# Kernel tuning notes

Hardware: AMD Instinct MI355X
Metric: run time of the kernel (lower is better)

Reference implementation:

```python
import jax, jax.numpy as jnp
import numpy as np

N_NODES = 100000
N_EDGES = 1600000
D_FEAT = 64
COS_EPS = 1e-8  # torch.nn.functional.cosine_similarity default eps


def setup_inputs() -> dict:
    key = jax.random.key(0)
    k1, k2 = jax.random.split(key)
    features = jax.random.normal(k1, (N_NODES, D_FEAT), dtype=jnp.float32)
    edge_index = jax.random.randint(k2, (2, N_EDGES), 0, N_NODES, dtype=jnp.int64)
    return {"features": features, "edge_index": edge_index}


def _mean_agg(h, src, dst, n_nodes):
    # copy_u: message = h[src]; fn.mean: per-dst mean over incoming messages
    msg_sum = jax.ops.segment_sum(h[src], dst, num_segments=n_nodes)  # [N, d]
    deg = jax.ops.segment_sum(jnp.ones(src.shape, h.dtype), dst, num_segments=n_nodes)  # [N]
    deg = deg[:, None]
    # nodes with zero in-degree get 0 (DGL mean semantics)
    return jnp.where(deg > 0, msg_sum / jnp.maximum(deg, 1.0), 0.0)


def reference(features, edge_index):
    src, dst = edge_index[0], edge_index[1]
    n = features.shape[0]
    x1 = _mean_agg(features, src, dst, n)   # gcn1
    x2 = _mean_agg(x1, src, dst, n)         # gcn2
    # cosine similarity along feature dim
    dot = jnp.sum(x1 * x2, axis=-1)
    n1 = jnp.linalg.norm(x1, axis=-1)
    n2 = jnp.linalg.norm(x2, axis=-1)
    cos = dot / jnp.maximum(n1 * n2, COS_EPS)
    w = cos[:, None]
    return w * x2 + (1.0 - w) * x1
```

## Files before the change

kernel.cpp:

```cpp
#include <hip/hip_runtime.h>
#include <hip/hip_fp16.h>
#include <math.h>

#define N_NODES 100000
#define N_EDGES 1600000
#define D_FEAT  64

#define NPB     256
#define NBC     ((N_NODES + NPB - 1) / NPB)
#define F1_WGS  512
#define NV4     (N_EDGES / 4)
#define CHUNK_V ((NV4 + F1_WGS - 1) / F1_WGS)
#define STAGE_CAP 8192
#define CASTN   ((N_NODES * D_FEAT) / 4)
#define CAST_BLOCKS ((CASTN + 255) / 256)


__device__ __forceinline__ uint4 pack8(const float* v) {
    __half2 h0 = __floats2half2_rn(v[0], v[1]);
    __half2 h1 = __floats2half2_rn(v[2], v[3]);
    __half2 h2 = __floats2half2_rn(v[4], v[5]);
    __half2 h3 = __floats2half2_rn(v[6], v[7]);
    uint4 st;
    st.x = *(unsigned*)&h0; st.y = *(unsigned*)&h1;
    st.z = *(unsigned*)&h2; st.w = *(unsigned*)&h3;
    return st;
}

__device__ __forceinline__ void unp8(uint4 u, float* a) {
    { __half2 h = *(__half2*)&u.x; float2 f = __half22float2(h); a[0]=f.x; a[1]=f.y; }
    { __half2 h = *(__half2*)&u.y; float2 f = __half22float2(h); a[2]=f.x; a[3]=f.y; }
    { __half2 h = *(__half2*)&u.z; float2 f = __half22float2(h); a[4]=f.x; a[5]=f.y; }
    { __half2 h = *(__half2*)&u.w; float2 f = __half22float2(h); a[6]=f.x; a[7]=f.y; }
}

__device__ __forceinline__ int block_excl_scan_512(int v, int t, int* wsum) {
    int lane = t & 63, wv = t >> 6;
    int incl = v;
    #pragma unroll
    for (int m = 1; m < 64; m <<= 1) {
        int o = __shfl_up(incl, m);
        if (lane >= m) incl += o;
    }
    if (lane == 63) wsum[wv] = incl;
    __syncthreads();
    int prefix = 0;
    #pragma unroll
    for (int j = 0; j < 8; j++)
        if (j < wv) prefix += wsum[j];
    return prefix + incl - v;
}


__global__ void cast_and_hist(const float* __restrict__ feat,
                              __half* __restrict__ feat_h,
                              const int4* __restrict__ dst4,
                              int* __restrict__ percnt) {
    if (blockIdx.x >= F1_WGS) {
        int i = (blockIdx.x - F1_WGS) * 256 + threadIdx.x;
        if (i < CASTN) {
            float4 v = ((const float4*)feat)[i];
            __half2 h0 = __floats2half2_rn(v.x, v.y);
            __half2 h1 = __floats2half2_rn(v.z, v.w);
            uint2 st;
            st.x = *(unsigned*)&h0;
            st.y = *(unsigned*)&h1;
            ((uint2*)feat_h)[i] = st;
        }
        return;
    }
    __shared__ int cnt[NBC];
    for (int i = threadIdx.x; i < NBC; i += blockDim.x) cnt[i] = 0;
    __syncthreads();
    int i0 = blockIdx.x * CHUNK_V;
    int i1 = min(i0 + CHUNK_V, NV4);
    for (int i = i0 + threadIdx.x; i < i1; i += blockDim.x) {
        int4 d = dst4[i];
        atomicAdd(&cnt[d.x >> 8], 1);
        atomicAdd(&cnt[d.y >> 8], 1);
        atomicAdd(&cnt[d.z >> 8], 1);
        atomicAdd(&cnt[d.w >> 8], 1);
    }
    __syncthreads();
    for (int i = threadIdx.x; i < NBC; i += blockDim.x)
        percnt[i * F1_WGS + blockIdx.x] = cnt[i];
}


__global__ __launch_bounds__(F1_WGS) void bucket_colscan(
        int* __restrict__ percnt, int* __restrict__ bhist) {
    __shared__ int wsum[8];
    int b = blockIdx.x, t = threadIdx.x;
    int v = percnt[b * F1_WGS + t];
    int excl = block_excl_scan_512(v, t, wsum);
    percnt[b * F1_WGS + t] = excl;
    if (t == F1_WGS - 1) bhist[b] = excl + v;
}

__global__ __launch_bounds__(F1_WGS) void bucketize(
        const int4* __restrict__ src4,
        const int4* __restrict__ dst4,
        const int* __restrict__ bhist,
        const int* __restrict__ percnt,
        unsigned int* __restrict__ tmp1) {
    __shared__ int base[NBC];
    __shared__ int cur[NBC];
    __shared__ int wsum[8];
    int wg = blockIdx.x, t = threadIdx.x;
    int v = (t < NBC) ? bhist[t] : 0;
    int excl = block_excl_scan_512(v, t, wsum);
    if (t < NBC) {
        base[t] = excl + percnt[t * F1_WGS + wg];
        cur[t] = 0;
    }
    __syncthreads();
    int i0 = wg * CHUNK_V;
    int i1 = min(i0 + CHUNK_V, NV4);
    for (int i = i0 + t; i < i1; i += F1_WGS) {
        int4 d = dst4[i];
        int4 s = src4[i];
        {
            int b = d.x >> 8; int r = atomicAdd(&cur[b], 1);
            tmp1[base[b] + r] = ((unsigned)s.x << 8) | (unsigned)(d.x & 255);
        }
        {
            int b = d.y >> 8; int r = atomicAdd(&cur[b], 1);
            tmp1[base[b] + r] = ((unsigned)s.y << 8) | (unsigned)(d.y & 255);
        }
        {
            int b = d.z >> 8; int r = atomicAdd(&cur[b], 1);
            tmp1[base[b] + r] = ((unsigned)s.z << 8) | (unsigned)(d.z & 255);
        }
        {
            int b = d.w >> 8; int r = atomicAdd(&cur[b], 1);
            tmp1[base[b] + r] = ((unsigned)s.w << 8) | (unsigned)(d.w & 255);
        }
    }
}

__global__ __launch_bounds__(512) void bucket_csr(
        const unsigned int* __restrict__ tmp1,
        const int* __restrict__ bhist,
        int* __restrict__ offsets,
        int* __restrict__ csr_src) {
    __shared__ int cnt[NPB];
    __shared__ int off[NPB];
    __shared__ int wsum[8];
    __shared__ int stage[STAGE_CAP];
    __shared__ int sEbase, sEcnt;
    int b = blockIdx.x, t = threadIdx.x;

    {
        int v = (t < NBC) ? bhist[t] : 0;
        int ex = block_excl_scan_512(v, t, wsum);
        if (t == b) { sEbase = ex; sEcnt = v; }
    }
    if (t < NPB) cnt[t] = 0;
    __syncthreads();
    int ebase = sEbase;
    int ecnt  = sEcnt;
    int node0 = b * NPB;

    for (int i = t; i < ecnt; i += 512)
        atomicAdd(&cnt[tmp1[ebase + i] & 255], 1);
    __syncthreads();

    int v = (t < NPB) ? cnt[t] : 0;
    int excl = block_excl_scan_512(v, t, wsum);
    if (t < NPB) {
        off[t] = excl;
        cnt[t] = 0;
        if (node0 + t < N_NODES) offsets[node0 + t] = ebase + excl;
    }
    if (b == NBC - 1 && t == 0) offsets[N_NODES] = N_EDGES;
    __syncthreads();

    if (ecnt <= STAGE_CAP) {
        for (int i = t; i < ecnt; i += 512) {
            unsigned u = tmp1[ebase + i];
            int d = (int)(u & 255);
            int r = atomicAdd(&cnt[d], 1);
            stage[off[d] + r] = (int)(u >> 8);
        }
        __syncthreads();
        for (int i = t; i < ecnt; i += 512)
            csr_src[ebase + i] = stage[i];
    } else {
        for (int i = t; i < ecnt; i += 512) {
            unsigned u = tmp1[ebase + i];
            int d = (int)(u & 255);
            int r = atomicAdd(&cnt[d], 1);
            csr_src[ebase + off[d] + r] = (int)(u >> 8);
        }
    }
}


__global__ void gather1_kernel(const __half* __restrict__ feat_h,
                               const int* __restrict__ offsets,
                               const int* __restrict__ csr,
                               __half* __restrict__ x1_h) {
    __shared__ int scsr[4][64];
    int wv = threadIdx.x >> 6;
    int node = blockIdx.x * 4 + wv;
    if (node >= N_NODES) return;
    int lane = threadIdx.x & 63;
    int g = lane >> 3;
    int fid = (lane & 7) * 8;

    int base = offsets[node];
    int deg = offsets[node + 1] - base;

    if (lane < deg) scsr[wv][lane] = csr[base + lane];
    __builtin_amdgcn_wave_barrier();

    __half2 h0 = __float2half2_rn(0.f), h1 = h0, h2 = h0, h3 = h0;
    int dmax = min(deg, 64);
    for (int j = g; j < dmax; j += 8) {
        int s = scsr[wv][j];
        uint4 u = *(const uint4*)(feat_h + ((size_t)s << 6) + fid);
        h0 = __hadd2(h0, *(__half2*)&u.x);
        h1 = __hadd2(h1, *(__half2*)&u.y);
        h2 = __hadd2(h2, *(__half2*)&u.z);
        h3 = __hadd2(h3, *(__half2*)&u.w);
    }
    for (int j = 64 + g; j < deg; j += 8) {
        int s = csr[base + j];
        uint4 u = *(const uint4*)(feat_h + ((size_t)s << 6) + fid);
        h0 = __hadd2(h0, *(__half2*)&u.x);
        h1 = __hadd2(h1, *(__half2*)&u.y);
        h2 = __hadd2(h2, *(__half2*)&u.z);
        h3 = __hadd2(h3, *(__half2*)&u.w);
    }
    float acc[8];
    { float2 f = __half22float2(h0); acc[0]=f.x; acc[1]=f.y; }
    { float2 f = __half22float2(h1); acc[2]=f.x; acc[3]=f.y; }
    { float2 f = __half22float2(h2); acc[4]=f.x; acc[5]=f.y; }
    { float2 f = __half22float2(h3); acc[6]=f.x; acc[7]=f.y; }
    #pragma unroll
    for (int m = 8; m < 64; m <<= 1)
        #pragma unroll
        for (int t = 0; t < 8; t++)
            acc[t] += __shfl_xor(acc[t], m);

    if (lane < 8) {
        float inv = (deg > 0) ? 1.0f / (float)deg : 0.0f;
        float r[8];
        #pragma unroll
        for (int t = 0; t < 8; t++) r[t] = acc[t] * inv;
        *(uint4*)(x1_h + ((size_t)node << 6) + fid) = pack8(r);
    }
}

__global__ void gather2_finalize_kernel(const __half* __restrict__ x1_h,
                                        const int* __restrict__ offsets,
                                        const int* __restrict__ csr,
                                        float* __restrict__ out) {
    __shared__ int scsr[4][64];
    int wv = threadIdx.x >> 6;
    int node = blockIdx.x * 4 + wv;
    if (node >= N_NODES) return;
    int lane = threadIdx.x & 63;
    int g = lane >> 3;
    int fid = (lane & 7) * 8;

    int base = offsets[node];
    int deg = offsets[node + 1] - base;

    if (lane < deg) scsr[wv][lane] = csr[base + lane];
    __builtin_amdgcn_wave_barrier();

    __half2 h0 = __float2half2_rn(0.f), h1 = h0, h2 = h0, h3 = h0;
    int dmax = min(deg, 64);
    for (int j = g; j < dmax; j += 8) {
        int s = scsr[wv][j];
        uint4 u = *(const uint4*)(x1_h + ((size_t)s << 6) + fid);
        h0 = __hadd2(h0, *(__half2*)&u.x);
        h1 = __hadd2(h1, *(__half2*)&u.y);
        h2 = __hadd2(h2, *(__half2*)&u.z);
        h3 = __hadd2(h3, *(__half2*)&u.w);
    }
    for (int j = 64 + g; j < deg; j += 8) {
        int s = csr[base + j];
        uint4 u = *(const uint4*)(x1_h + ((size_t)s << 6) + fid);
        h0 = __hadd2(h0, *(__half2*)&u.x);
        h1 = __hadd2(h1, *(__half2*)&u.y);
        h2 = __hadd2(h2, *(__half2*)&u.z);
        h3 = __hadd2(h3, *(__half2*)&u.w);
    }
    float acc[8];
    { float2 f = __half22float2(h0); acc[0]=f.x; acc[1]=f.y; }
    { float2 f = __half22float2(h1); acc[2]=f.x; acc[3]=f.y; }
    { float2 f = __half22float2(h2); acc[4]=f.x; acc[5]=f.y; }
    { float2 f = __half22float2(h3); acc[6]=f.x; acc[7]=f.y; }
    #pragma unroll
    for (int m = 8; m < 64; m <<= 1)
        #pragma unroll
        for (int t = 0; t < 8; t++)
            acc[t] += __shfl_xor(acc[t], m);

    float inv = (deg > 0) ? 1.0f / (float)deg : 0.0f;
    float b[8], a[8];
    #pragma unroll
    for (int t = 0; t < 8; t++) b[t] = acc[t] * inv;

    uint4 ua = *(const uint4*)(x1_h + ((size_t)node << 6) + fid);
    unp8(ua, a);

    float dot = 0.f, nn1 = 0.f, nn2 = 0.f;
    #pragma unroll
    for (int t = 0; t < 8; t++) {
        dot += a[t] * b[t];
        nn1 += a[t] * a[t];
        nn2 += b[t] * b[t];
    }
    #pragma unroll
    for (int m = 1; m < 64; m <<= 1) {
        dot += __shfl_xor(dot, m);
        nn1 += __shfl_xor(nn1, m);
        nn2 += __shfl_xor(nn2, m);
    }
    dot *= 0.125f; nn1 *= 0.125f; nn2 *= 0.125f;

    float w = dot / fmaxf(sqrtf(nn1) * sqrtf(nn2), 1e-8f);
    if (lane < 8) {
        float omw = 1.0f - w;
        float4 r0, r1;
        r0.x = w*b[0] + omw*a[0]; r0.y = w*b[1] + omw*a[1];
        r0.z = w*b[2] + omw*a[2]; r0.w = w*b[3] + omw*a[3];
        r1.x = w*b[4] + omw*a[4]; r1.y = w*b[5] + omw*a[5];
        r1.z = w*b[6] + omw*a[6]; r1.w = w*b[7] + omw*a[7];
        float* po = out + ((size_t)node << 6) + fid;
        *(float4*)po = r0;
        *(float4*)(po + 4) = r1;
    }
}


extern "C" void kernel_launch(void* const* d_in, const int* in_sizes, int n_in,
                              void* d_out, int out_size, void* d_ws, size_t ws_size,
                              hipStream_t stream) {
    const float* feat = (const float*)d_in[0];
    const int*   eidx = (const int*)d_in[1];
    const int4*  src4 = (const int4*)eidx;
    const int4*  dst4 = (const int4*)(eidx + N_EDGES);

    __half*       feat_h  = (__half*)d_ws;
    __half*       x1_h    = feat_h + (size_t)N_NODES * D_FEAT;
    unsigned int* tmp1    = (unsigned int*)(x1_h + (size_t)N_NODES * D_FEAT);
    int*          csr_src = (int*)(tmp1 + N_EDGES);
    int*          offsets = csr_src + N_EDGES;
    int*          percnt  = offsets + (N_NODES + 1);
    int*          bhist   = percnt + NBC * F1_WGS;
    float*        out     = (float*)d_out;

    cast_and_hist <<<F1_WGS + CAST_BLOCKS, 256, 0, stream>>>(feat, feat_h, dst4, percnt);
    bucket_colscan<<<NBC, F1_WGS, 0, stream>>>(percnt, bhist);
    bucketize     <<<F1_WGS, F1_WGS, 0, stream>>>(src4, dst4, bhist, percnt, tmp1);
    bucket_csr    <<<NBC, 512, 0, stream>>>(tmp1, bhist, offsets, csr_src);

    const int BLK = 256;
    int nblocks = (N_NODES + 3) / 4;
    gather1_kernel<<<nblocks, BLK, 0, stream>>>(feat_h, offsets, csr_src, x1_h);
    gather2_finalize_kernel<<<nblocks, BLK, 0, stream>>>(x1_h, offsets, csr_src, out);
}
```

Before: 196.9 us.

## Map eight nodes per wavefront in gather kernels, removing cross-group shuffle reductions

```diff
diff --git a/kernel.cpp b/kernel.cpp
--- a/kernel.cpp
+++ b/kernel.cpp
@@ -14,6 +14,8 @@
 #define STAGE_CAP 8192
 #define CASTN   ((N_NODES * D_FEAT) / 4)
 #define CAST_BLOCKS ((CASTN + 255) / 256)
+
+#define GCAP    68
 
 
 __device__ __forceinline__ uint4 pack8(const float* v) {
@@ -196,115 +198,102 @@
 }
 
 
-__global__ void gather1_kernel(const __half* __restrict__ feat_h,
-                               const int* __restrict__ offsets,
-                               const int* __restrict__ csr,
-                               __half* __restrict__ x1_h) {
-    __shared__ int scsr[4][64];
-    int wv = threadIdx.x >> 6;
-    int node = blockIdx.x * 4 + wv;
-    if (node >= N_NODES) return;
+__global__ __launch_bounds__(256) void gather1_kernel(
+        const __half* __restrict__ feat_h,
+        const int* __restrict__ offsets,
+        const int* __restrict__ csr,
+        __half* __restrict__ x1_h) {
+    __shared__ int snbr[4][8][GCAP];
+    int wv   = threadIdx.x >> 6;
     int lane = threadIdx.x & 63;
-    int g = lane >> 3;
-    int fid = (lane & 7) * 8;
+    int g    = lane >> 3;
+    int fl   = lane & 7;
+    int node = (blockIdx.x * 4 + wv) * 8 + g;
 
     int base = offsets[node];
-    int deg = offsets[node + 1] - base;
-
-    if (lane < deg) scsr[wv][lane] = csr[base + lane];
+    int deg  = offsets[node + 1] - base;
+    int dcap = min(deg, GCAP);
+
+    int* my = snbr[wv][g];
+    for (int j = fl; j < dcap; j += 8)
+        my[j] = csr[base + j];
     __builtin_amdgcn_wave_barrier();
 
     __half2 h0 = __float2half2_rn(0.f), h1 = h0, h2 = h0, h3 = h0;
-    int dmax = min(deg, 64);
-    for (int j = g; j < dmax; j += 8) {
-        int s = scsr[wv][j];
-        uint4 u = *(const uint4*)(feat_h + ((size_t)s << 6) + fid);
+    const __half* fb = feat_h + (fl << 3);
+    for (int j = 0; j < dcap; ++j) {
+        int s = my[j];
+        uint4 u = *(const uint4*)(fb + ((size_t)s << 6));
         h0 = __hadd2(h0, *(__half2*)&u.x);
         h1 = __hadd2(h1, *(__half2*)&u.y);
         h2 = __hadd2(h2, *(__half2*)&u.z);
         h3 = __hadd2(h3, *(__half2*)&u.w);
     }
-    for (int j = 64 + g; j < deg; j += 8) {
+    for (int j = GCAP; j < deg; ++j) {
         int s = csr[base + j];
-        uint4 u = *(const uint4*)(feat_h + ((size_t)s << 6) + fid);
+        uint4 u = *(const uint4*)(fb + ((size_t)s << 6));
         h0 = __hadd2(h0, *(__half2*)&u.x);
         h1 = __hadd2(h1, *(__half2*)&u.y);
         h2 = __hadd2(h2, *(__half2*)&u.z);
         h3 = __hadd2(h3, *(__half2*)&u.w);
     }
-    float acc[8];
-    { float2 f = __half22float2(h0); acc[0]=f.x; acc[1]=f.y; }
-    { float2 f = __half22float2(h1); acc[2]=f.x; acc[3]=f.y; }
-    { float2 f = __half22float2(h2); acc[4]=f.x; acc[5]=f.y; }
-    { float2 f = __half22float2(h3); acc[6]=f.x; acc[7]=f.y; }
-    #pragma unroll
-    for (int m = 8; m < 64; m <<= 1)
-        #pragma unroll
-        for (int t = 0; t < 8; t++)
-            acc[t] += __shfl_xor(acc[t], m);
-
-    if (lane < 8) {
-        float inv = (deg > 0) ? 1.0f / (float)deg : 0.0f;
-        float r[8];
-        #pragma unroll
-        for (int t = 0; t < 8; t++) r[t] = acc[t] * inv;
-        *(uint4*)(x1_h + ((size_t)node << 6) + fid) = pack8(r);
-    }
-}
-
-__global__ void gather2_finalize_kernel(const __half* __restrict__ x1_h,
-                                        const int* __restrict__ offsets,
-                                        const int* __restrict__ csr,
-                                        float* __restrict__ out) {
-    __shared__ int scsr[4][64];
-    int wv = threadIdx.x >> 6;
-    int node = blockIdx.x * 4 + wv;
-    if (node >= N_NODES) return;
+    float invf = (deg > 0) ? __builtin_amdgcn_rcpf((float)deg) : 0.0f;
+    float r[8];
+    { float2 f = __half22float2(h0); r[0]=f.x*invf; r[1]=f.y*invf; }
+    { float2 f = __half22float2(h1); r[2]=f.x*invf; r[3]=f.y*invf; }
+    { float2 f = __half22float2(h2); r[4]=f.x*invf; r[5]=f.y*invf; }
+    { float2 f = __half22float2(h3); r[6]=f.x*invf; r[7]=f.y*invf; }
+    *(uint4*)(x1_h + ((size_t)node << 6) + (fl << 3)) = pack8(r);
+}
+
+__global__ __launch_bounds__(256) void gather2_finalize_kernel(
+        const __half* __restrict__ x1_h,
+        const int* __restrict__ offsets,
+        const int* __restrict__ csr,
+        float* __restrict__ out) {
+    __shared__ int snbr[4][8][GCAP];
+    int wv   = threadIdx.x >> 6;
     int lane = threadIdx.x & 63;
-    int g = lane >> 3;
-    int fid = (lane & 7) * 8;
+    int g    = lane >> 3;
+    int fl   = lane & 7;
+    int node = (blockIdx.x * 4 + wv) * 8 + g;
 
     int base = offsets[node];
-    int deg = offsets[node + 1] - base;
-
-    if (lane < deg) scsr[wv][lane] = csr[base + lane];
+    int deg  = offsets[node + 1] - base;
+    int dcap = min(deg, GCAP);
+
+    int* my = snbr[wv][g];
+    for (int j = fl; j < dcap; j += 8)
+        my[j] = csr[base + j];
     __builtin_amdgcn_wave_barrier();
 
     __half2 h0 = __float2half2_rn(0.f), h1 = h0, h2 = h0, h3 = h0;
-    int dmax = min(deg, 64);
-    for (int j = g; j < dmax; j += 8) {
-        int s = scsr[wv][j];
-        uint4 u = *(const uint4*)(x1_h + ((size_t)s << 6) + fid);
+    const __half* fb = x1_h + (fl << 3);
+    for (int j = 0; j < dcap; ++j) {
+        int s = my[j];
+        uint4 u = *(const uint4*)(fb + ((size_t)s << 6));
         h0 = __hadd2(h0, *(__half2*)&u.x);
         h1 = __hadd2(h1, *(__half2*)&u.y);
         h2 = __hadd2(h2, *(__half2*)&u.z);
         h3 = __hadd2(h3, *(__half2*)&u.w);
     }
-    for (int j = 64 + g; j < deg; j += 8) {
+    for (int j = GCAP; j < deg; ++j) {
         int s = csr[base + j];
-        uint4 u = *(const uint4*)(x1_h + ((size_t)s << 6) + fid);
+        uint4 u = *(const uint4*)(fb + ((size_t)s << 6));
         h0 = __hadd2(h0, *(__half2*)&u.x);
         h1 = __hadd2(h1, *(__half2*)&u.y);
         h2 = __hadd2(h2, *(__half2*)&u.z);
         h3 = __hadd2(h3, *(__half2*)&u.w);
     }
-    float acc[8];
-    { float2 f = __half22float2(h0); acc[0]=f.x; acc[1]=f.y; }
-    { float2 f = __half22float2(h1); acc[2]=f.x; acc[3]=f.y; }
-    { float2 f = __half22float2(h2); acc[4]=f.x; acc[5]=f.y; }
-    { float2 f = __half22float2(h3); acc[6]=f.x; acc[7]=f.y; }
-    #pragma unroll
-    for (int m = 8; m < 64; m <<= 1)
-        #pragma unroll
-        for (int t = 0; t < 8; t++)
-            acc[t] += __shfl_xor(acc[t], m);
-
-    float inv = (deg > 0) ? 1.0f / (float)deg : 0.0f;
-    float b[8], a[8];
-    #pragma unroll
-    for (int t = 0; t < 8; t++) b[t] = acc[t] * inv;
-
-    uint4 ua = *(const uint4*)(x1_h + ((size_t)node << 6) + fid);
+    float invf = (deg > 0) ? __builtin_amdgcn_rcpf((float)deg) : 0.0f;
+    float b[8];
+    { float2 f = __half22float2(h0); b[0]=f.x*invf; b[1]=f.y*invf; }
+    { float2 f = __half22float2(h1); b[2]=f.x*invf; b[3]=f.y*invf; }
+    { float2 f = __half22float2(h2); b[4]=f.x*invf; b[5]=f.y*invf; }
+    { float2 f = __half22float2(h3); b[6]=f.x*invf; b[7]=f.y*invf; }
+
+    float a[8];
+    uint4 ua = *(const uint4*)(x1_h + ((size_t)node << 6) + (fl << 3));
     unp8(ua, a);
 
     float dot = 0.f, nn1 = 0.f, nn2 = 0.f;
@@ -315,25 +304,24 @@
         nn2 += b[t] * b[t];
     }
     #pragma unroll
-    for (int m = 1; m < 64; m <<= 1) {
+    for (int m = 1; m < 8; m <<= 1) {
         dot += __shfl_xor(dot, m);
         nn1 += __shfl_xor(nn1, m);
         nn2 += __shfl_xor(nn2, m);
     }
-    dot *= 0.125f; nn1 *= 0.125f; nn2 *= 0.125f;
-
-    float w = dot / fmaxf(sqrtf(nn1) * sqrtf(nn2), 1e-8f);
-    if (lane < 8) {
-        float omw = 1.0f - w;
-        float4 r0, r1;
-        r0.x = w*b[0] + omw*a[0]; r0.y = w*b[1] + omw*a[1];
-        r0.z = w*b[2] + omw*a[2]; r0.w = w*b[3] + omw*a[3];
-        r1.x = w*b[4] + omw*a[4]; r1.y = w*b[5] + omw*a[5];
-        r1.z = w*b[6] + omw*a[6]; r1.w = w*b[7] + omw*a[7];
-        float* po = out + ((size_t)node << 6) + fid;
-        *(float4*)po = r0;
-        *(float4*)(po + 4) = r1;
-    }
+
+    float denom = fmaxf(__builtin_amdgcn_sqrtf(nn1 * nn2), 1e-8f);
+    float w = dot * __builtin_amdgcn_rcpf(denom);
+    float omw = 1.0f - w;
+
+    float4 r0, r1;
+    r0.x = w*b[0] + omw*a[0]; r0.y = w*b[1] + omw*a[1];
+    r0.z = w*b[2] + omw*a[2]; r0.w = w*b[3] + omw*a[3];
+    r1.x = w*b[4] + omw*a[4]; r1.y = w*b[5] + omw*a[5];
+    r1.z = w*b[6] + omw*a[6]; r1.w = w*b[7] + omw*a[7];
+    float* po = out + ((size_t)node << 6) + (fl << 3);
+    *(float4*)po = r0;
+    *(float4*)(po + 4) = r1;
 }
 
 
@@ -360,7 +348,7 @@
     bucket_csr    <<<NBC, 512, 0, stream>>>(tmp1, bhist, offsets, csr_src);
 
     const int BLK = 256;
-    int nblocks = (N_NODES + 3) / 4;
+    int nblocks = N_NODES / 32;
     gather1_kernel<<<nblocks, BLK, 0, stream>>>(feat_h, offsets, csr_src, x1_h);
     gather2_finalize_kernel<<<nblocks, BLK, 0, stream>>>(x1_h, offsets, csr_src, out);
 }
```

Result: faster. 164.7 us (-16.3%).
